# Performance work log

Measured on AMD Instinct MI355X. Metric: run time of the kernel, lower is better.

Reference implementation:

```python
import jax, jax.numpy as jnp
import numpy as np

B, T, C = 2, 2048, 1024
H = 16
D = C // H  # head size 64


def setup_inputs() -> dict:
    key = jax.random.key(0)
    ks = jax.random.split(key, 9)
    s = 0.02
    return {
        "x": jax.random.normal(ks[0], (B, T, C), dtype=jnp.float32),
        "Wq": jax.random.normal(ks[1], (C, C), dtype=jnp.float32) * s,
        "bq": jnp.zeros((C,), dtype=jnp.float32),
        "Wk": jax.random.normal(ks[2], (C, C), dtype=jnp.float32) * s,
        "bk": jnp.zeros((C,), dtype=jnp.float32),
        "Wv": jax.random.normal(ks[3], (C, C), dtype=jnp.float32) * s,
        "bv": jnp.zeros((C,), dtype=jnp.float32),
        "Wo": jax.random.normal(ks[4], (C, C), dtype=jnp.float32) * s,
        "bo": jnp.zeros((C,), dtype=jnp.float32),
    }


def reference(x, Wq, bq, Wk, bk, Wv, bv, Wo, bo):
    b, t, c = x.shape
    scale = 1.0 / jnp.sqrt(jnp.asarray(D, dtype=x.dtype))
    # projections (torch Linear: x @ W.T + b), then split heads -> [B,H,T,D]
    def split_heads(y):
        return y.reshape(b, t, H, D).transpose(0, 2, 1, 3)
    q = split_heads(x @ Wq.T + bq)
    k = split_heads(x @ Wk.T + bk)
    v = split_heads(x @ Wv.T + bv)
    # scores [B,H,T,T], causal mask (triu above diagonal = -inf)
    attn = jnp.einsum("bhqd,bhkd->bhqk", q, k) * scale
    causal = jnp.tril(jnp.ones((t, t), dtype=bool))  # True = keep
    attn = jnp.where(causal[None, None], attn, -jnp.inf)
    attn = jax.nn.softmax(attn, axis=-1)
    # dropout p=0.0 -> identity
    y = jnp.einsum("bhqk,bhkd->bhqd", attn, v)
    y = y.transpose(0, 2, 1, 3).reshape(b, t, c)
    return y @ Wo.T + bo
```

## Files before the change

kernel.cpp:

```cpp
#include <hip/hip_runtime.h>
#include <hip/hip_bf16.h>
#include <stdint.h>
#include <stddef.h>


typedef __bf16 bf16;
typedef __attribute__((ext_vector_type(8))) __bf16 bf16x8;
typedef __attribute__((ext_vector_type(4))) __bf16 bf16x4;
typedef __attribute__((ext_vector_type(4))) float floatx4;

#define MFMA_16x16x32(A, B, C) __builtin_amdgcn_mfma_f32_16x16x32_bf16(A, B, C, 0, 0, 0)

static constexpr int T_SEQ = 2048;
static constexpr int CDIM  = 1024;

__device__ __forceinline__ void gl2lds16(const bf16* g, bf16* l) {
  __builtin_amdgcn_global_load_lds(
      (const __attribute__((address_space(1))) uint32_t*)g,
      (__attribute__((address_space(3))) uint32_t*)l, 16, 0, 0);
}

__global__ __launch_bounds__(256) void convert_kernel(
    const float* __restrict__ x, const float* __restrict__ Wq,
    const float* __restrict__ Wk, const float* __restrict__ Wv,
    const float* __restrict__ Wo,
    bf16* __restrict__ Xb, bf16* __restrict__ Wqkvb, bf16* __restrict__ Wob) {
  size_t i = ((size_t)blockIdx.x * 256 + threadIdx.x) * 4;
  const float* src;
  bf16* dst;
  size_t off;
  if (i < 4194304) {
    src = x; dst = Xb; off = i;
  } else {
    size_t r = i - 4194304;
    int wsel = (int)(r >> 20);
    off = r & 1048575;
    src = (wsel == 0) ? Wq : (wsel == 1) ? Wk : (wsel == 2) ? Wv : Wo;
    dst = (wsel < 3) ? (Wqkvb + ((size_t)wsel << 20)) : Wob;
  }
  float4 v = *(const float4*)(src + off);
  bf16x4 o;
  o[0] = (bf16)v.x; o[1] = (bf16)v.y; o[2] = (bf16)v.z; o[3] = (bf16)v.w;
  *(bf16x4*)(dst + off) = o;
}

__global__ __launch_bounds__(256) void gemm_qkv(
    const bf16* __restrict__ Xb, const bf16* __restrict__ Wqkvb,
    const float* __restrict__ bq, const float* __restrict__ bk,
    const float* __restrict__ bv,
    bf16* __restrict__ Qb, bf16* __restrict__ Kb, bf16* __restrict__ Vtb) {
  __shared__ __align__(16) bf16 smem[12288];
  bf16* As = smem;
  bf16* Bs = smem + 4096;
  bf16* Cs = smem;

  const int bM = blockIdx.x & 63;
  const int bN = blockIdx.x >> 6;
  const int tid = threadIdx.x;
  const int w = tid >> 6, l = tid & 63;
  const int wm = w & 1, wn = w >> 1;
  const int lr = l >> 3, cl = l & 7;
  const int fr = l & 15, q4 = l >> 4;
  const int fc = fr;

  floatx4 acc[2][4];
#pragma unroll
  for (int mi = 0; mi < 2; ++mi)
#pragma unroll
    for (int ni = 0; ni < 4; ++ni)
#pragma unroll
      for (int r = 0; r < 4; ++r) acc[mi][ni][r] = 0.0f;

  for (int k0 = 0; k0 < CDIM; k0 += 64) {
#pragma unroll
    for (int i = 0; i < 2; ++i) {
      int row = i * 32 + w * 8 + lr;
      int cg = cl ^ (row & 7);
      gl2lds16(Xb + (size_t)(bM * 64 + row) * CDIM + k0 + cg * 8,
               As + row * 64 + cl * 8);
    }
#pragma unroll
    for (int i = 0; i < 4; ++i) {
      int row = i * 32 + w * 8 + lr;
      int cg = cl ^ (row & 7);
      gl2lds16(Wqkvb + (size_t)(bN * 128 + row) * CDIM + k0 + cg * 8,
               Bs + row * 64 + cl * 8);
    }
    __syncthreads();
#pragma unroll
    for (int kk = 0; kk < 2; ++kk) {
      const int cgk = kk * 4 + q4;
      bf16x8 af[2], bfr[4];
#pragma unroll
      for (int mi = 0; mi < 2; ++mi) {
        int row = wm * 32 + mi * 16 + fr;
        af[mi] = *(const bf16x8*)(As + row * 64 + (cgk ^ (row & 7)) * 8);
      }
#pragma unroll
      for (int ni = 0; ni < 4; ++ni) {
        int row = wn * 64 + ni * 16 + fr;
        bfr[ni] = *(const bf16x8*)(Bs + row * 64 + (cgk ^ (row & 7)) * 8);
      }
#pragma unroll
      for (int mi = 0; mi < 2; ++mi)
#pragma unroll
        for (int ni = 0; ni < 4; ++ni)
          acc[mi][ni] = MFMA_16x16x32(af[mi], bfr[ni], acc[mi][ni]);
    }
    __syncthreads();
  }

  const int seg = bN >> 3;
  const float QSCALE = 0.125f * 1.44269504089f;
  const float* bp = (seg == 0) ? bq : (seg == 1) ? bk : bv;

#pragma unroll
  for (int ni = 0; ni < 4; ++ni) {
    int jl = wn * 64 + ni * 16 + fc;
    float bias = bp[(bN * 128 + jl) & 1023];
#pragma unroll
    for (int mi = 0; mi < 2; ++mi)
#pragma unroll
      for (int r = 0; r < 4; ++r) {
        int ttl = wm * 32 + mi * 16 + q4 * 4 + r;
        float val = acc[mi][ni][r] + bias;
        if (seg == 0) val *= QSCALE;
        int addr = (seg == 2) ? jl * 72 + ttl : ttl * 136 + jl;
        Cs[addr] = (bf16)val;
      }
  }
  __syncthreads();

  if (seg < 2) {
    bf16* basep = (seg == 0) ? Qb : Kb;
    const int chunk = tid & 15;
    const int rb = (tid >> 4) * 4;
#pragma unroll
    for (int u = 0; u < 4; ++u) {
      int maj = rb + u;
      bf16x8 vdat = *(const bf16x8*)(Cs + maj * 136 + chunk * 8);
      int n = bM * 64 + maj;
      int b = n >> 11, tt = n & 2047;
      int j = bN * 128 + chunk * 8;
      int h = (j >> 6) & 15, d = j & 63;
      *(bf16x8*)(basep + (((size_t)(b * 16 + h) * T_SEQ + tt) << 6) + d) = vdat;
    }
  } else {
    const int chunk = tid & 7;
    const int rb = (tid >> 3) * 4;
#pragma unroll
    for (int u = 0; u < 4; ++u) {
      int maj = rb + u;
      bf16x8 vdat = *(const bf16x8*)(Cs + maj * 72 + chunk * 8);
      int j = bN * 128 + maj;
      int h = (j >> 6) & 15, d = j & 63;
      int n0 = bM * 64 + chunk * 8;
      int b = n0 >> 11, tt0 = n0 & 2047;
      *(bf16x8*)(Vtb + ((size_t)(b * 16 + h) * 64 + d) * T_SEQ + tt0) = vdat;
    }
  }
}

__global__ __launch_bounds__(256) void flash_attn(
    const bf16* __restrict__ Qb, const bf16* __restrict__ Kb,
    const bf16* __restrict__ Vtb, bf16* __restrict__ Ao) {
  __shared__ __align__(16) bf16 Ks[64 * 64];
  __shared__ __align__(16) bf16 Vs[64 * 64];
  __shared__ __align__(16) bf16 Ps[4][16 * 72];

  const int bh = blockIdx.x;
  const int ymap = blockIdx.y;
  const int a = ymap & 7, kq = ymap >> 3;
  const int qt = (kq == 0) ? 31 - a : (kq == 1) ? 16 + a : (kq == 2) ? 15 - a : a;
  const int b = bh >> 4, h = bh & 15;
  const int tid = threadIdx.x;
  const int w = tid >> 6, l = tid & 63;
  const int fc = l & 15, q4 = l >> 4;
  const int lr = l >> 3, cl = l & 7;

  const bf16* Qg = Qb + (size_t)bh * T_SEQ * 64;
  const bf16* Kg = Kb + (size_t)bh * T_SEQ * 64;
  const bf16* Vg = Vtb + (size_t)bh * 64 * T_SEQ;

  const int qrow = qt * 64 + w * 16 + fc;
  bf16x8 qf[2];
  qf[0] = *(const bf16x8*)(Qg + (size_t)qrow * 64 + q4 * 8);
  qf[1] = *(const bf16x8*)(Qg + (size_t)qrow * 64 + 32 + q4 * 8);

  bf16x8 ones;
#pragma unroll
  for (int i = 0; i < 8; ++i) ones[i] = (bf16)1.0f;

  floatx4 o[4];
  floatx4 lacc;
#pragma unroll
  for (int ds = 0; ds < 4; ++ds)
#pragma unroll
    for (int r = 0; r < 4; ++r) o[ds][r] = 0.0f;
#pragma unroll
  for (int r = 0; r < 4; ++r) lacc[r] = 0.0f;

  for (int kv = 0; kv <= qt; ++kv) {
    const int kvbase = kv * 64;
#pragma unroll
    for (int i = 0; i < 2; ++i) {
      int row = i * 32 + w * 8 + lr;
      int cg = cl ^ (row & 7);
      gl2lds16(Kg + (size_t)(kvbase + row) * 64 + cg * 8, Ks + row * 64 + cl * 8);
      gl2lds16(Vg + (size_t)row * T_SEQ + kvbase + cg * 8, Vs + row * 64 + cl * 8);
    }
    __syncthreads();

    floatx4 s[4];
#pragma unroll
    for (int ni = 0; ni < 4; ++ni)
#pragma unroll
      for (int r = 0; r < 4; ++r) s[ni][r] = 0.0f;
#pragma unroll
    for (int kk = 0; kk < 2; ++kk) {
      const int cgk = kk * 4 + q4;
#pragma unroll
      for (int ni = 0; ni < 4; ++ni) {
        int row = ni * 16 + fc;
        bf16x8 kf = *(const bf16x8*)(Ks + row * 64 + (cgk ^ (row & 7)) * 8);
        s[ni] = MFMA_16x16x32(qf[kk], kf, s[ni]);
      }
    }

    if (kv == qt) {
      int qc = w * 16 + q4 * 4;
#pragma unroll
      for (int ni = 0; ni < 4; ++ni)
#pragma unroll
        for (int r = 0; r < 4; ++r) {
          int kc = ni * 16 + fc;
          float pv = (kc > qc + r) ? 0.0f : __builtin_amdgcn_exp2f(s[ni][r]);
          Ps[w][(q4 * 4 + r) * 72 + ni * 16 + fc] = (bf16)pv;
        }
    } else {
#pragma unroll
      for (int ni = 0; ni < 4; ++ni)
#pragma unroll
        for (int r = 0; r < 4; ++r)
          Ps[w][(q4 * 4 + r) * 72 + ni * 16 + fc] =
              (bf16)__builtin_amdgcn_exp2f(s[ni][r]);
    }

#pragma unroll
    for (int kk = 0; kk < 2; ++kk) {
      bf16x8 pf = *(const bf16x8*)(&Ps[w][fc * 72 + kk * 32 + q4 * 8]);
      const int cgk = kk * 4 + q4;
#pragma unroll
      for (int ds = 0; ds < 4; ++ds) {
        int row = ds * 16 + fc;
        bf16x8 vf = *(const bf16x8*)(Vs + row * 64 + (cgk ^ (row & 7)) * 8);
        o[ds] = MFMA_16x16x32(pf, vf, o[ds]);
      }
      lacc = MFMA_16x16x32(pf, ones, lacc);
    }
    __syncthreads();
  }

  float inv[4];
#pragma unroll
  for (int r = 0; r < 4; ++r) inv[r] = __builtin_amdgcn_rcpf(lacc[r]);
#pragma unroll
  for (int ds = 0; ds < 4; ++ds)
#pragma unroll
    for (int r = 0; r < 4; ++r) {
      int tt = qt * 64 + w * 16 + q4 * 4 + r;
      int col = h * 64 + ds * 16 + fc;
      Ao[((size_t)(b * T_SEQ + tt) << 10) + col] = (bf16)(o[ds][r] * inv[r]);
    }
}

__global__ __launch_bounds__(256) void gemm_out(
    const bf16* __restrict__ Ab, const bf16* __restrict__ Wob,
    const float* __restrict__ bo, float* __restrict__ Y) {
  __shared__ __align__(16) bf16 As[64 * 64];
  __shared__ __align__(16) bf16 Bs[64 * 64];
  const int bM = blockIdx.x & 63;
  const int bN = blockIdx.x >> 6;
  const int tid = threadIdx.x;
  const int w = tid >> 6, l = tid & 63;
  const int wm = w & 1, wn = w >> 1;
  const int lr = l >> 3, cl = l & 7;
  const int fr = l & 15, q4 = l >> 4;
  const int fc = fr;

  floatx4 acc[2][2];
#pragma unroll
  for (int mi = 0; mi < 2; ++mi)
#pragma unroll
    for (int ni = 0; ni < 2; ++ni)
#pragma unroll
      for (int r = 0; r < 4; ++r) acc[mi][ni][r] = 0.0f;

  for (int k0 = 0; k0 < CDIM; k0 += 64) {
#pragma unroll
    for (int i = 0; i < 2; ++i) {
      int row = i * 32 + w * 8 + lr;
      int cg = cl ^ (row & 7);
      gl2lds16(Ab + (size_t)(bM * 64 + row) * CDIM + k0 + cg * 8,
               As + row * 64 + cl * 8);
      gl2lds16(Wob + (size_t)(bN * 64 + row) * CDIM + k0 + cg * 8,
               Bs + row * 64 + cl * 8);
    }
    __syncthreads();
#pragma unroll
    for (int kk = 0; kk < 2; ++kk) {
      const int cgk = kk * 4 + q4;
      bf16x8 af[2], bfr[2];
#pragma unroll
      for (int mi = 0; mi < 2; ++mi) {
        int row = wm * 32 + mi * 16 + fr;
        af[mi] = *(const bf16x8*)(As + row * 64 + (cgk ^ (row & 7)) * 8);
      }
#pragma unroll
      for (int ni = 0; ni < 2; ++ni) {
        int row = wn * 32 + ni * 16 + fr;
        bfr[ni] = *(const bf16x8*)(Bs + row * 64 + (cgk ^ (row & 7)) * 8);
      }
#pragma unroll
      for (int mi = 0; mi < 2; ++mi)
#pragma unroll
        for (int ni = 0; ni < 2; ++ni)
          acc[mi][ni] = MFMA_16x16x32(af[mi], bfr[ni], acc[mi][ni]);
    }
    __syncthreads();
  }

#pragma unroll
  for (int ni = 0; ni < 2; ++ni) {
    int j = bN * 64 + wn * 32 + ni * 16 + fc;
    float bias = bo[j];
#pragma unroll
    for (int mi = 0; mi < 2; ++mi)
#pragma unroll
      for (int r = 0; r < 4; ++r) {
        int n = bM * 64 + wm * 32 + mi * 16 + q4 * 4 + r;
        Y[(size_t)n * CDIM + j] = acc[mi][ni][r] + bias;
      }
  }
}

extern "C" void kernel_launch(void* const* d_in, const int* in_sizes, int n_in,
                              void* d_out, int out_size, void* d_ws, size_t ws_size,
                              hipStream_t stream) {
  const float* x  = (const float*)d_in[0];
  const float* Wq = (const float*)d_in[1];
  const float* bq = (const float*)d_in[2];
  const float* Wk = (const float*)d_in[3];
  const float* bk = (const float*)d_in[4];
  const float* Wv = (const float*)d_in[5];
  const float* bv = (const float*)d_in[6];
  const float* Wo = (const float*)d_in[7];
  const float* bo = (const float*)d_in[8];
  float* Y = (float*)d_out;

  char* ws = (char*)d_ws;
  const size_t MB = 1024 * 1024;
  bf16* Xb    = (bf16*)(ws + 0);
  bf16* Wqkvb = (bf16*)(ws + 8 * MB);
  bf16* Wob   = (bf16*)(ws + 14 * MB);
  bf16* Qb    = (bf16*)(ws + 16 * MB);
  bf16* Kb    = (bf16*)(ws + 24 * MB);
  bf16* Vtb   = (bf16*)(ws + 32 * MB);
  bf16* Ao    = Xb;

  convert_kernel<<<8192, 256, 0, stream>>>(x, Wq, Wk, Wv, Wo, Xb, Wqkvb, Wob);
  gemm_qkv<<<64 * 24, 256, 0, stream>>>(Xb, Wqkvb, bq, bk, bv, Qb, Kb, Vtb);
  flash_attn<<<dim3(32, 32), 256, 0, stream>>>(Qb, Kb, Vtb, Ao);
  gemm_out<<<64 * 16, 256, 0, stream>>>(Ao, Wob, bo, Y);
}
```

Baseline: 181.7 us.

## Load K/V fragments directly from global memory, drop LDS staging and barriers

The flash attention kernel no longer stages K and V tiles through shared memory with global_load_lds. Each wave now reads its MFMA operand fragments straight from global memory, relying on L1/L2 caching for reuse across the four waves. This removes both __syncthreads per KV tile and most LDS use. P is double-buffered per wave, and launch bounds now request 4 blocks per CU to raise occupancy. The cost is redundant global/L2 traffic (each wave re-reads the same K/V) and more exposed load latency without explicit prefetch.

Result: slower. 262.9 us (+44.6%).

```diff
diff --git a/kernel.cpp b/kernel.cpp
--- a/kernel.cpp
+++ b/kernel.cpp
@@ -161,12 +161,10 @@
   }
 }
 
-__global__ __launch_bounds__(256) void flash_attn(
+__global__ __launch_bounds__(256, 4) void flash_attn(
     const bf16* __restrict__ Qb, const bf16* __restrict__ Kb,
     const bf16* __restrict__ Vtb, bf16* __restrict__ Ao) {
-  __shared__ __align__(16) bf16 Ks[64 * 64];
-  __shared__ __align__(16) bf16 Vs[64 * 64];
-  __shared__ __align__(16) bf16 Ps[4][16 * 72];
+  __shared__ __align__(16) bf16 Ps[4][2][16 * 72];
 
   const int bh = blockIdx.x;
   const int ymap = blockIdx.y;
@@ -176,7 +174,6 @@
   const int tid = threadIdx.x;
   const int w = tid >> 6, l = tid & 63;
   const int fc = l & 15, q4 = l >> 4;
-  const int lr = l >> 3, cl = l & 7;
 
   const bf16* Qg = Qb + (size_t)bh * T_SEQ * 64;
   const bf16* Kg = Kb + (size_t)bh * T_SEQ * 64;
@@ -187,6 +184,9 @@
   qf[0] = *(const bf16x8*)(Qg + (size_t)qrow * 64 + q4 * 8);
   qf[1] = *(const bf16x8*)(Qg + (size_t)qrow * 64 + 32 + q4 * 8);
 
+  const bf16* Kl = Kg + (size_t)fc * 64 + q4 * 8;
+  const bf16* Vl = Vg + (size_t)fc * T_SEQ + q4 * 8;
+
   bf16x8 ones;
 #pragma unroll
   for (int i = 0; i < 8; ++i) ones[i] = (bf16)1.0f;
@@ -200,16 +200,12 @@
 #pragma unroll
   for (int r = 0; r < 4; ++r) lacc[r] = 0.0f;
 
+  bf16* PsW0 = &Ps[w][0][0];
+  bf16* PsW1 = &Ps[w][1][0];
+
   for (int kv = 0; kv <= qt; ++kv) {
-    const int kvbase = kv * 64;
-#pragma unroll
-    for (int i = 0; i < 2; ++i) {
-      int row = i * 32 + w * 8 + lr;
-      int cg = cl ^ (row & 7);
-      gl2lds16(Kg + (size_t)(kvbase + row) * 64 + cg * 8, Ks + row * 64 + cl * 8);
-      gl2lds16(Vg + (size_t)row * T_SEQ + kvbase + cg * 8, Vs + row * 64 + cl * 8);
-    }
-    __syncthreads();
+    const size_t kvb = (size_t)kv * 64;
+    bf16* PsW = (kv & 1) ? PsW1 : PsW0;
 
     floatx4 s[4];
 #pragma unroll
@@ -218,11 +214,9 @@
       for (int r = 0; r < 4; ++r) s[ni][r] = 0.0f;
 #pragma unroll
     for (int kk = 0; kk < 2; ++kk) {
-      const int cgk = kk * 4 + q4;
 #pragma unroll
       for (int ni = 0; ni < 4; ++ni) {
-        int row = ni * 16 + fc;
-        bf16x8 kf = *(const bf16x8*)(Ks + row * 64 + (cgk ^ (row & 7)) * 8);
+        bf16x8 kf = *(const bf16x8*)(Kl + (kvb + ni * 16) * 64 + kk * 32);
         s[ni] = MFMA_16x16x32(qf[kk], kf, s[ni]);
       }
     }
@@ -235,30 +229,27 @@
         for (int r = 0; r < 4; ++r) {
           int kc = ni * 16 + fc;
           float pv = (kc > qc + r) ? 0.0f : __builtin_amdgcn_exp2f(s[ni][r]);
-          Ps[w][(q4 * 4 + r) * 72 + ni * 16 + fc] = (bf16)pv;
+          PsW[(q4 * 4 + r) * 72 + ni * 16 + fc] = (bf16)pv;
         }
     } else {
 #pragma unroll
       for (int ni = 0; ni < 4; ++ni)
 #pragma unroll
         for (int r = 0; r < 4; ++r)
-          Ps[w][(q4 * 4 + r) * 72 + ni * 16 + fc] =
+          PsW[(q4 * 4 + r) * 72 + ni * 16 + fc] =
               (bf16)__builtin_amdgcn_exp2f(s[ni][r]);
     }
 
 #pragma unroll
     for (int kk = 0; kk < 2; ++kk) {
-      bf16x8 pf = *(const bf16x8*)(&Ps[w][fc * 72 + kk * 32 + q4 * 8]);
-      const int cgk = kk * 4 + q4;
+      bf16x8 pf = *(const bf16x8*)(&PsW[fc * 72 + kk * 32 + q4 * 8]);
 #pragma unroll
       for (int ds = 0; ds < 4; ++ds) {
-        int row = ds * 16 + fc;
-        bf16x8 vf = *(const bf16x8*)(Vs + row * 64 + (cgk ^ (row & 7)) * 8);
+        bf16x8 vf = *(const bf16x8*)(Vl + (size_t)(ds * 16) * T_SEQ + kvb + kk * 32);
         o[ds] = MFMA_16x16x32(pf, vf, o[ds]);
       }
       lacc = MFMA_16x16x32(pf, ones, lacc);
     }
-    __syncthreads();
   }
 
   float inv[4];
```
